# Performance work log

Measured on AMD Instinct MI355X. Metric: run time of the kernel, lower is better.

Reference implementation:

```python
import jax, jax.numpy as jnp
import numpy as np

N = 50000      # nodes
E = 400000     # edges per meta-path
P = 3          # meta-paths
H = 4          # attention heads
D = 32         # hidden_size per head
IN = 128       # in_size = 86 + 42
HD = H * D     # 128
NEG_SLOPE = 0.2


def setup_inputs() -> dict:
    key = jax.random.key(0)
    ks = jax.random.split(key, 13)
    return {
        "h": jax.random.normal(ks[0], (N, 86), dtype=jnp.float32),
        "c_ineigh_feature": jax.random.normal(ks[1], (N, 20, 42), dtype=jnp.float32),
        "fa_w1": jax.random.normal(ks[2], (42, 16), dtype=jnp.float32) * 0.1,
        "fa_b1": jnp.zeros((16,), dtype=jnp.float32),
        "fa_w2": jax.random.normal(ks[3], (16, 1), dtype=jnp.float32) * 0.1,
        "gat_W": jax.random.normal(ks[4], (P, IN, HD), dtype=jnp.float32) * 0.05,
        "attn_l": jax.random.normal(ks[5], (P, H, D), dtype=jnp.float32) * 0.1,
        "attn_r": jax.random.normal(ks[6], (P, H, D), dtype=jnp.float32) * 0.1,
        "sa_w1": jax.random.normal(ks[7], (HD, 128), dtype=jnp.float32) * 0.1,
        "sa_b1": jnp.zeros((128,), dtype=jnp.float32),
        "sa_w2": jax.random.normal(ks[8], (128, 1), dtype=jnp.float32) * 0.1,
        "src": jax.random.randint(ks[9], (P, E), 0, N, dtype=jnp.int32),
        "dst": jax.random.randint(ks[10], (P, E), 0, N, dtype=jnp.int32),
    }


def _gat_conv(x, W, a_l, a_r, s, d):
    """DGL-style GATConv (feat_drop=attn_drop=0, eval mode), activation=elu."""
    feat = (x @ W).reshape(N, H, D)               # [N,H,D]
    el = (feat * a_l).sum(-1)                     # [N,H]
    er = (feat * a_r).sum(-1)                     # [N,H]
    e = el[s] + er[d]                             # [E,H]
    e = jnp.where(e > 0, e, NEG_SLOPE * e)        # leaky_relu(0.2)
    # edge softmax over incoming edges of each dst node
    m = jax.ops.segment_max(e, d, num_segments=N)
    m = jax.lax.stop_gradient(jnp.where(jnp.isfinite(m), m, 0.0))
    ee = jnp.exp(e - m[d])                        # [E,H]
    z = jax.ops.segment_sum(ee, d, num_segments=N)
    alpha = ee / z[d]                             # [E,H]
    msg = alpha[:, :, None] * feat[s]             # [E,H,D]
    out = jax.ops.segment_sum(msg, d, num_segments=N)  # [N,H,D]
    return jax.nn.elu(out).reshape(N, HD)


def reference(h, c_ineigh_feature, fa_w1, fa_b1, fa_w2, gat_W, attn_l, attn_r,
              sa_w1, sa_b1, sa_w2, src, dst):
    # FeatureAttention over the 42-dim neighbor features
    w = jnp.tanh(c_ineigh_feature @ fa_w1 + fa_b1) @ fa_w2   # [N,20,1]
    beta = jax.nn.softmax(w, axis=1)
    c_emb = (beta * c_ineigh_feature).sum(1)                 # [N,42]
    x = jnp.concatenate([h, c_emb], axis=1)                  # [N,128]

    # One GATConv per meta-path
    embs = [_gat_conv(x, gat_W[p], attn_l[p], attn_r[p], src[p], dst[p])
            for p in range(P)]
    z = jnp.stack(embs, axis=1)                              # [N,P,HD]

    # SemanticAttention across meta-paths
    wsem = (jnp.tanh(z @ sa_w1 + sa_b1) @ sa_w2).mean(0)     # [P,1]
    bsem = jax.nn.softmax(wsem, axis=0)                      # [P,1]
    return (bsem[None] * z).sum(1)                           # [N,HD]
```

## Files before the change

kernel.cpp:

```cpp
#include <hip/hip_runtime.h>
#include <hip/hip_bf16.h>

#define NN 50000
#define EE 400000
#define PP 3
#define NBLK 196

__device__ __forceinline__ float eluf(float v) {
    return v > 0.f ? v : (expf(v) - 1.f);
}

__global__ __launch_bounds__(256) void k_featattn(
    const float* __restrict__ h, const float* __restrict__ c,
    const float* __restrict__ w1, const float* __restrict__ b1,
    const float* __restrict__ w2, float* __restrict__ x)
{
    __shared__ float sC[16 * 840];
    __shared__ float sW1[42 * 16];
    __shared__ float sB1[16];
    __shared__ float sW2[16];
    const int tid = threadIdx.x;
    const int n0 = blockIdx.x * 16;

    for (int i = tid; i < 672; i += 256) sW1[i] = w1[i];
    if (tid < 16) { sB1[tid] = b1[tid]; sW2[tid] = w2[tid]; }

    const float4* c4 = (const float4*)(c + (size_t)n0 * 840);
    float4* sC4 = (float4*)sC;
    for (int i = tid; i < 3360; i += 256) sC4[i] = c4[i];
    __syncthreads();

    const int j  = tid & 15;
    const int nn = tid >> 4;
    const float* myC = sC + nn * 840;
    const float bj = sB1[j], w2j = sW2[j];

    float part[20];
    for (int r = 0; r < 20; ++r) {
        float acc = bj;
        const float* row = myC + r * 42;
        #pragma unroll
        for (int i = 0; i < 42; ++i) acc += row[i] * sW1[i * 16 + j];
        part[r] = tanhf(acc) * w2j;
    }
    #pragma unroll
    for (int r = 0; r < 20; ++r) {
        float v = part[r];
        v += __shfl_xor(v, 1);
        v += __shfl_xor(v, 2);
        v += __shfl_xor(v, 4);
        v += __shfl_xor(v, 8);
        part[r] = v;
    }
    float m = part[0];
    #pragma unroll
    for (int r = 1; r < 20; ++r) m = fmaxf(m, part[r]);
    float s = 0.f;
    #pragma unroll
    for (int r = 0; r < 20; ++r) { part[r] = expf(part[r] - m); s += part[r]; }
    const float inv = 1.f / s;

    float e0 = 0.f, e1 = 0.f, e2 = 0.f;
    #pragma unroll
    for (int r = 0; r < 20; ++r) {
        const float b = part[r] * inv;
        const float* row = myC + r * 42;
        e0 += b * row[j];
        e1 += b * row[j + 16];
        if (j < 10) e2 += b * row[j + 32];
    }
    const int n = n0 + nn;
    float* xr = x + (size_t)n * 128;
    xr[86 + j]      = e0;
    xr[86 + j + 16] = e1;
    if (j < 10) xr[86 + j + 32] = e2;

    for (int i = tid; i < 16 * 86; i += 256) {
        const int node = i / 86, col = i % 86;
        x[(size_t)(n0 + node) * 128 + col] = h[(size_t)(n0 + node) * 86 + col];
    }
}

__global__ __launch_bounds__(256) void k_gat_gemm(
    const float* __restrict__ x, const float* __restrict__ W,
    const float* __restrict__ attn_l, const float* __restrict__ attn_r,
    float* __restrict__ feat, float* __restrict__ el, float* __restrict__ er)
{
    __shared__ float sX[64 * 128];
    const int tid = threadIdx.x;
    const int p  = blockIdx.y;
    const int n0 = blockIdx.x * 64;

    float4* sX4 = (float4*)sX;
    for (int i = tid; i < 2048; i += 256) {
        const int row = i >> 5, c4 = i & 31;
        float4 v = make_float4(0.f, 0.f, 0.f, 0.f);
        if (n0 + row < NN) v = ((const float4*)(x + (size_t)(n0 + row) * 128))[c4];
        sX4[i] = v;
    }
    __syncthreads();

    const int tc = tid & 31;
    const int tr = tid >> 5;
    const float* Wp = W + (size_t)p * 128 * 128;

    float acc[8][4];
    for (int r = 0; r < 8; ++r)
        for (int q = 0; q < 4; ++q) acc[r][q] = 0.f;

    #pragma unroll 4
    for (int k = 0; k < 128; ++k) {
        const float4 wv = ((const float4*)(Wp + k * 128))[tc];
        #pragma unroll
        for (int r = 0; r < 8; ++r) {
            const float xv = sX[(tr * 8 + r) * 128 + k];
            acc[r][0] += xv * wv.x;
            acc[r][1] += xv * wv.y;
            acc[r][2] += xv * wv.z;
            acc[r][3] += xv * wv.w;
        }
    }

    float al[4], ar[4];
    {
        const float* alp = attn_l + p * 128 + tc * 4;
        const float* arp = attn_r + p * 128 + tc * 4;
        for (int q = 0; q < 4; ++q) { al[q] = alp[q]; ar[q] = arp[q]; }
    }
    const int hh = tc >> 3;
    for (int r = 0; r < 8; ++r) {
        const int n = n0 + tr * 8 + r;
        const bool ok = n < NN;
        if (ok) {
            const float4 v = make_float4(acc[r][0], acc[r][1], acc[r][2], acc[r][3]);
            ((float4*)(feat + (size_t)(p * NN + n) * 128))[tc] = v;
        }
        float pl = acc[r][0]*al[0] + acc[r][1]*al[1] + acc[r][2]*al[2] + acc[r][3]*al[3];
        float pr = acc[r][0]*ar[0] + acc[r][1]*ar[1] + acc[r][2]*ar[2] + acc[r][3]*ar[3];
        pl += __shfl_xor(pl, 1); pl += __shfl_xor(pl, 2); pl += __shfl_xor(pl, 4);
        pr += __shfl_xor(pr, 1); pr += __shfl_xor(pr, 2); pr += __shfl_xor(pr, 4);
        if (ok && (tc & 7) == 0) {
            el[(size_t)(p * NN + n) * 4 + hh] = pl;
            er[(size_t)(p * NN + n) * 4 + hh] = pr;
        }
    }
}

__global__ __launch_bounds__(256) void k_hist(
    const int* __restrict__ dst, int* __restrict__ deg)
{
    const int p = blockIdx.y;
    const int e = blockIdx.x * 256 + threadIdx.x;
    if (e < EE) atomicAdd(&deg[p * NN + dst[p * EE + e]], 1);
}

__global__ __launch_bounds__(256) void k_partial(
    const int* __restrict__ deg, int* __restrict__ psum)
{
    __shared__ int s[256];
    const int p = blockIdx.y;
    const int i = blockIdx.x * 256 + threadIdx.x;
    s[threadIdx.x] = (i < NN) ? deg[p * NN + i] : 0;
    __syncthreads();
    for (int off = 128; off > 0; off >>= 1) {
        if (threadIdx.x < off) s[threadIdx.x] += s[threadIdx.x + off];
        __syncthreads();
    }
    if (threadIdx.x == 0) psum[p * NBLK + blockIdx.x] = s[0];
}

__global__ void k_scanpsum(int* __restrict__ psum)
{
    const int p = blockIdx.x;
    if (threadIdx.x == 0) {
        int run = 0;
        for (int i = 0; i < NBLK; ++i) {
            int t = psum[p * NBLK + i];
            psum[p * NBLK + i] = run;
            run += t;
        }
    }
}

__global__ __launch_bounds__(256) void k_scanfinal(
    const int* __restrict__ deg, const int* __restrict__ psum,
    int* __restrict__ row_start, int* __restrict__ cursor)
{
    __shared__ int s[256];
    const int p = blockIdx.y, t = threadIdx.x;
    const int i = blockIdx.x * 256 + t;
    const int v = (i < NN) ? deg[p * NN + i] : 0;
    s[t] = v;
    __syncthreads();
    for (int off = 1; off < 256; off <<= 1) {
        int xv = 0;
        if (t >= off) xv = s[t - off];
        __syncthreads();
        s[t] += xv;
        __syncthreads();
    }
    const int excl = s[t] - v + psum[p * NBLK + blockIdx.x];
    if (i < NN) {
        row_start[p * (NN + 1) + i] = excl;
        cursor[p * NN + i] = excl;
        if (i == NN - 1) row_start[p * (NN + 1) + NN] = excl + v;
    }
}

__global__ __launch_bounds__(256) void k_scatter(
    const int* __restrict__ src, const int* __restrict__ dst,
    const float* __restrict__ el, const float* __restrict__ er,
    int* __restrict__ cursor, int* __restrict__ s_src, float* __restrict__ s_ee)
{
    const int p = blockIdx.y;
    const int e = blockIdx.x * 256 + threadIdx.x;
    if (e >= EE) return;
    const int s = src[p * EE + e];
    const int d = dst[p * EE + e];
    const float4 a = ((const float4*)el)[p * NN + s];
    const float4 b = ((const float4*)er)[p * NN + d];
    float4 o;
    {
        float t0 = a.x + b.x, t1 = a.y + b.y, t2 = a.z + b.z, t3 = a.w + b.w;
        t0 = t0 > 0.f ? t0 : 0.2f * t0;
        t1 = t1 > 0.f ? t1 : 0.2f * t1;
        t2 = t2 > 0.f ? t2 : 0.2f * t2;
        t3 = t3 > 0.f ? t3 : 0.2f * t3;
        o = make_float4(expf(t0), expf(t1), expf(t2), expf(t3));
    }
    const int slot = atomicAdd(&cursor[p * NN + d], 1);
    s_src[p * EE + slot] = s;
    ((float4*)s_ee)[p * EE + slot] = o;
}

__global__ __launch_bounds__(256) void k_agg(
    const int* __restrict__ row_start, const int* __restrict__ s_src,
    const float* __restrict__ s_ee, const float* __restrict__ feat,
    float* __restrict__ z)
{
    const int p = blockIdx.y;
    const int w = threadIdx.x >> 6;
    const int lane = threadIdx.x & 63;
    const int n = blockIdx.x * 4 + w;
    if (n >= NN) return;
    const int st = row_start[p * (NN + 1) + n];
    const int en = row_start[p * (NN + 1) + n + 1];

    const bool lo = lane < 32;
    const int* ss = s_src + (size_t)p * EE;
    const float4* ee4 = (const float4*)s_ee + (size_t)p * EE;
    const float* fbase = feat + (size_t)p * NN * 128;

    float acc0 = 0.f, acc1 = 0.f, za = 0.f, zb = 0.f;
    for (int i = st; i < en; ++i) {
        const int sn = ss[i];
        const float4 e4 = ee4[i];
        const float ea = lo ? e4.x : e4.y;
        const float eb = lo ? e4.z : e4.w;
        const float* f = fbase + (size_t)sn * 128;
        acc0 += ea * f[lane];
        acc1 += eb * f[lane + 64];
        za += ea;
        zb += eb;
    }
    float v0 = 0.f, v1 = 0.f;
    if (en > st) { v0 = acc0 / za; v1 = acc1 / zb; }
    v0 = v0 > 0.f ? v0 : (expf(v0) - 1.f);
    v1 = v1 > 0.f ? v1 : (expf(v1) - 1.f);
    const size_t o = (size_t)(p * NN + n) * 128;
    z[o + lane] = v0;
    z[o + 64 + lane] = v1;
}

__global__ __launch_bounds__(256) void k_sem_score(
    const float* __restrict__ z, const float* __restrict__ w1,
    const float* __restrict__ b1, const float* __restrict__ w2,
    float* __restrict__ wsem)
{
    __shared__ float sZ[64 * 128];
    __shared__ float sPart[8];
    const int tid = threadIdx.x;
    const int p  = blockIdx.y;
    const int n0 = blockIdx.x * 64;

    float4* sZ4 = (float4*)sZ;
    for (int i = tid; i < 2048; i += 256) {
        const int row = i >> 5, c4 = i & 31;
        float4 v = make_float4(0.f, 0.f, 0.f, 0.f);
        if (n0 + row < NN)
            v = ((const float4*)(z + (size_t)(p * NN + n0 + row) * 128))[c4];
        sZ4[i] = v;
    }
    __syncthreads();

    const int tc = tid & 31;
    const int tr = tid >> 5;

    float acc[8][4];
    for (int r = 0; r < 8; ++r)
        for (int q = 0; q < 4; ++q) acc[r][q] = 0.f;

    #pragma unroll 4
    for (int k = 0; k < 128; ++k) {
        const float4 wv = ((const float4*)(w1 + k * 128))[tc];
        #pragma unroll
        for (int r = 0; r < 8; ++r) {
            const float zv = sZ[(tr * 8 + r) * 128 + k];
            acc[r][0] += zv * wv.x;
            acc[r][1] += zv * wv.y;
            acc[r][2] += zv * wv.z;
            acc[r][3] += zv * wv.w;
        }
    }

    float bb[4], ww[4];
    for (int q = 0; q < 4; ++q) { bb[q] = b1[tc * 4 + q]; ww[q] = w2[tc * 4 + q]; }

    float local = 0.f;
    for (int r = 0; r < 8; ++r) {
        float pr = 0.f;
        for (int q = 0; q < 4; ++q) pr += tanhf(acc[r][q] + bb[q]) * ww[q];
        pr += __shfl_xor(pr, 1);
        pr += __shfl_xor(pr, 2);
        pr += __shfl_xor(pr, 4);
        pr += __shfl_xor(pr, 8);
        pr += __shfl_xor(pr, 16);
        if (tc == 0 && (n0 + tr * 8 + r) < NN) local += pr;
    }
    if (tc == 0) sPart[tr] = local;
    __syncthreads();
    if (tid == 0) {
        float t = 0.f;
        for (int i = 0; i < 8; ++i) t += sPart[i];
        atomicAdd(&wsem[p], t);
    }
}

__global__ void k_bsem(const float* __restrict__ wsem, float* __restrict__ bsem)
{
    if (threadIdx.x == 0 && blockIdx.x == 0) {
        float w[PP];
        for (int p = 0; p < PP; ++p) w[p] = wsem[p] / (float)NN;
        float m = fmaxf(w[0], fmaxf(w[1], w[2]));
        float s = 0.f;
        for (int p = 0; p < PP; ++p) { w[p] = expf(w[p] - m); s += w[p]; }
        for (int p = 0; p < PP; ++p) bsem[p] = w[p] / s;
    }
}

__global__ __launch_bounds__(256) void k_final(
    const float* __restrict__ z, const float* __restrict__ bsem,
    float* __restrict__ out)
{
    const int i = blockIdx.x * 256 + threadIdx.x;
    if (i >= NN * 128) return;
    const float b0 = bsem[0], b1 = bsem[1], b2 = bsem[2];
    const float v0 = z[i];
    const float v1 = z[(size_t)NN * 128 + i];
    const float v2 = z[(size_t)2 * NN * 128 + i];
    out[i] = b0 * v0 + b1 * v1 + b2 * v2;
}

extern "C" void kernel_launch(void* const* d_in, const int* in_sizes, int n_in,
                              void* d_out, int out_size, void* d_ws, size_t ws_size,
                              hipStream_t stream) {
    const float* h      = (const float*)d_in[0];
    const float* c      = (const float*)d_in[1];
    const float* fa_w1  = (const float*)d_in[2];
    const float* fa_b1  = (const float*)d_in[3];
    const float* fa_w2  = (const float*)d_in[4];
    const float* gat_W  = (const float*)d_in[5];
    const float* attn_l = (const float*)d_in[6];
    const float* attn_r = (const float*)d_in[7];
    const float* sa_w1  = (const float*)d_in[8];
    const float* sa_b1  = (const float*)d_in[9];
    const float* sa_w2  = (const float*)d_in[10];
    const int*   src    = (const int*)d_in[11];
    const int*   dst    = (const int*)d_in[12];
    float* out = (float*)d_out;

    float* ws = (float*)d_ws;
    float* x    = ws;
    int*   s_src = (int*)x;
    float* s_ee  = x + 1200000;
    float* feat = x + 6400000;
    float* el   = feat + 19200000;
    float* er   = el + 600000;
    float* z    = er + 600000;
    int*   row_start = (int*)(z + 19200000);
    int*   cursor    = row_start + 150003;
    int*   psum      = cursor + 150000;
    int*   deg       = psum + 588;
    float* wsem      = (float*)(deg + 150000);
    float* bsem      = wsem + 4;

    hipMemsetAsync(deg, 0, (size_t)(150000 + 4) * sizeof(float), stream);

    k_featattn<<<NN / 16, 256, 0, stream>>>(h, c, fa_w1, fa_b1, fa_w2, x);
    k_gat_gemm<<<dim3((NN + 63) / 64, PP), 256, 0, stream>>>(x, gat_W, attn_l, attn_r, feat, el, er);
    k_hist<<<dim3((EE + 255) / 256, PP), 256, 0, stream>>>(dst, deg);
    k_partial<<<dim3(NBLK, PP), 256, 0, stream>>>(deg, psum);
    k_scanpsum<<<PP, 64, 0, stream>>>(psum);
    k_scanfinal<<<dim3(NBLK, PP), 256, 0, stream>>>(deg, psum, row_start, cursor);
    k_scatter<<<dim3((EE + 255) / 256, PP), 256, 0, stream>>>(src, dst, el, er, cursor, s_src, s_ee);
    k_agg<<<dim3((NN + 3) / 4, PP), 256, 0, stream>>>(row_start, s_src, s_ee, feat, z);
    k_sem_score<<<dim3((NN + 63) / 64, PP), 256, 0, stream>>>(z, sa_w1, sa_b1, sa_w2, wsem);
    k_bsem<<<1, 64, 0, stream>>>(wsem, bsem);
    k_final<<<(NN * 128 + 255) / 256, 256, 0, stream>>>(z, bsem, out);
}
```

Baseline: 817.4 us.

## Store GAT features in bf16, split feature attention, vectorize GEMM inner loops

GAT projected features are rounded to bf16 on write and gathered as packed pairs in the aggregation kernel, halving the bytes read per edge; each lane now covers two adjacent columns of one head. Feature attention is split into a per-row score kernel with register tiling and a per-node softmax/embedding kernel, removing the large shared-memory staging of the neighbor tensor. The projection and semantic-score GEMMs read shared memory as float4 and unroll over k by four. Precision loss from bf16 features may slightly change outputs.

```diff
diff --git a/kernel.cpp b/kernel.cpp
--- a/kernel.cpp
+++ b/kernel.cpp
@@ -10,81 +10,117 @@
     return v > 0.f ? v : (expf(v) - 1.f);
 }
 
-__global__ __launch_bounds__(256) void k_featattn(
+__device__ __forceinline__ void fma4(float4& a, float s, const float4& w) {
+    a.x += s * w.x; a.y += s * w.y; a.z += s * w.z; a.w += s * w.w;
+}
+
+__device__ __forceinline__ unsigned short f2bf(float f) {
+    unsigned int u = __float_as_uint(f);
+    u = (u + 0x7FFFu + ((u >> 16) & 1u)) >> 16;
+    return (unsigned short)u;
+}
+
+__global__ __launch_bounds__(256) void k_fa_w(
+    const float* __restrict__ c, const float* __restrict__ w1,
+    const float* __restrict__ b1, const float* __restrict__ w2,
+    float* __restrict__ wout)
+{
+    __shared__ float sW1[42 * 16];
+    const int tid = threadIdx.x;
+    for (int i = tid; i < 672; i += 256) sW1[i] = w1[i];
+    __syncthreads();
+
+    const int t = blockIdx.x * 256 + tid;
+    if (t >= NN * 5) return;
+    const int n = t / 5;
+    const int q = t - 5 * n;
+
+    const float2* base = (const float2*)(c + (size_t)n * 840 + q * 168);
+    const float4* sW4 = (const float4*)sW1;
+
+    float4 acc[4][4];
+    #pragma unroll
+    for (int r = 0; r < 4; ++r)
+        #pragma unroll
+        for (int jq = 0; jq < 4; ++jq) acc[r][jq] = make_float4(0.f, 0.f, 0.f, 0.f);
+
+    #pragma unroll 3
+    for (int i2 = 0; i2 < 21; ++i2) {
+        const float4 wa0 = sW4[(2 * i2) * 4 + 0];
+        const float4 wa1 = sW4[(2 * i2) * 4 + 1];
+        const float4 wa2 = sW4[(2 * i2) * 4 + 2];
+        const float4 wa3 = sW4[(2 * i2) * 4 + 3];
+        const float4 wb0 = sW4[(2 * i2 + 1) * 4 + 0];
+        const float4 wb1 = sW4[(2 * i2 + 1) * 4 + 1];
+        const float4 wb2 = sW4[(2 * i2 + 1) * 4 + 2];
+        const float4 wb3 = sW4[(2 * i2 + 1) * 4 + 3];
+        #pragma unroll
+        for (int r = 0; r < 4; ++r) {
+            const float2 v = base[r * 21 + i2];
+            fma4(acc[r][0], v.x, wa0); fma4(acc[r][1], v.x, wa1);
+            fma4(acc[r][2], v.x, wa2); fma4(acc[r][3], v.x, wa3);
+            fma4(acc[r][0], v.y, wb0); fma4(acc[r][1], v.y, wb1);
+            fma4(acc[r][2], v.y, wb2); fma4(acc[r][3], v.y, wb3);
+        }
+    }
+
+    float4 bb[4], ww[4];
+    #pragma unroll
+    for (int jq = 0; jq < 4; ++jq) {
+        bb[jq] = ((const float4*)b1)[jq];
+        ww[jq] = ((const float4*)w2)[jq];
+    }
+    float* wo = wout + (size_t)n * 20 + q * 4;
+    #pragma unroll
+    for (int r = 0; r < 4; ++r) {
+        float s = 0.f;
+        #pragma unroll
+        for (int jq = 0; jq < 4; ++jq) {
+            s += tanhf(acc[r][jq].x + bb[jq].x) * ww[jq].x;
+            s += tanhf(acc[r][jq].y + bb[jq].y) * ww[jq].y;
+            s += tanhf(acc[r][jq].z + bb[jq].z) * ww[jq].z;
+            s += tanhf(acc[r][jq].w + bb[jq].w) * ww[jq].w;
+        }
+        wo[r] = s;
+    }
+}
+
+__global__ __launch_bounds__(256) void k_fa_emb(
     const float* __restrict__ h, const float* __restrict__ c,
-    const float* __restrict__ w1, const float* __restrict__ b1,
-    const float* __restrict__ w2, float* __restrict__ x)
-{
-    __shared__ float sC[16 * 840];
-    __shared__ float sW1[42 * 16];
-    __shared__ float sB1[16];
-    __shared__ float sW2[16];
-    const int tid = threadIdx.x;
-    const int n0 = blockIdx.x * 16;
-
-    for (int i = tid; i < 672; i += 256) sW1[i] = w1[i];
-    if (tid < 16) { sB1[tid] = b1[tid]; sW2[tid] = w2[tid]; }
-
-    const float4* c4 = (const float4*)(c + (size_t)n0 * 840);
-    float4* sC4 = (float4*)sC;
-    for (int i = tid; i < 3360; i += 256) sC4[i] = c4[i];
-    __syncthreads();
-
-    const int j  = tid & 15;
-    const int nn = tid >> 4;
-    const float* myC = sC + nn * 840;
-    const float bj = sB1[j], w2j = sW2[j];
-
-    float part[20];
-    for (int r = 0; r < 20; ++r) {
-        float acc = bj;
-        const float* row = myC + r * 42;
-        #pragma unroll
-        for (int i = 0; i < 42; ++i) acc += row[i] * sW1[i * 16 + j];
-        part[r] = tanhf(acc) * w2j;
-    }
-    #pragma unroll
-    for (int r = 0; r < 20; ++r) {
-        float v = part[r];
-        v += __shfl_xor(v, 1);
-        v += __shfl_xor(v, 2);
-        v += __shfl_xor(v, 4);
-        v += __shfl_xor(v, 8);
-        part[r] = v;
-    }
-    float m = part[0];
-    #pragma unroll
-    for (int r = 1; r < 20; ++r) m = fmaxf(m, part[r]);
+    const float* __restrict__ w, float* __restrict__ x)
+{
+    const int wid = threadIdx.x >> 6, lane = threadIdx.x & 63;
+    const int n = blockIdx.x * 4 + wid;
+    if (n >= NN) return;
+
+    const float* wn = w + (size_t)n * 20;
+    float wv[20];
+    #pragma unroll
+    for (int r = 0; r < 20; ++r) wv[r] = wn[r];
+    float m = wv[0];
+    #pragma unroll
+    for (int r = 1; r < 20; ++r) m = fmaxf(m, wv[r]);
     float s = 0.f;
     #pragma unroll
-    for (int r = 0; r < 20; ++r) { part[r] = expf(part[r] - m); s += part[r]; }
+    for (int r = 0; r < 20; ++r) { wv[r] = expf(wv[r] - m); s += wv[r]; }
     const float inv = 1.f / s;
 
-    float e0 = 0.f, e1 = 0.f, e2 = 0.f;
-    #pragma unroll
-    for (int r = 0; r < 20; ++r) {
-        const float b = part[r] * inv;
-        const float* row = myC + r * 42;
-        e0 += b * row[j];
-        e1 += b * row[j + 16];
-        if (j < 10) e2 += b * row[j + 32];
-    }
-    const int n = n0 + nn;
-    float* xr = x + (size_t)n * 128;
-    xr[86 + j]      = e0;
-    xr[86 + j + 16] = e1;
-    if (j < 10) xr[86 + j + 32] = e2;
-
-    for (int i = tid; i < 16 * 86; i += 256) {
-        const int node = i / 86, col = i % 86;
-        x[(size_t)(n0 + node) * 128 + col] = h[(size_t)(n0 + node) * 86 + col];
-    }
+    if (lane < 42) {
+        const float* cn = c + (size_t)n * 840;
+        float acc = 0.f;
+        #pragma unroll
+        for (int r = 0; r < 20; ++r) acc += wv[r] * cn[r * 42 + lane];
+        x[(size_t)n * 128 + 86 + lane] = acc * inv;
+    }
+    x[(size_t)n * 128 + lane] = h[(size_t)n * 86 + lane];
+    if (lane < 22)
+        x[(size_t)n * 128 + 64 + lane] = h[(size_t)n * 86 + 64 + lane];
 }
 
 __global__ __launch_bounds__(256) void k_gat_gemm(
     const float* __restrict__ x, const float* __restrict__ W,
     const float* __restrict__ attn_l, const float* __restrict__ attn_r,
-    float* __restrict__ feat, float* __restrict__ el, float* __restrict__ er)
+    unsigned short* __restrict__ featb, float* __restrict__ el, float* __restrict__ er)
 {
     __shared__ float sX[64 * 128];
     const int tid = threadIdx.x;
@@ -102,41 +138,44 @@
 
     const int tc = tid & 31;
     const int tr = tid >> 5;
-    const float* Wp = W + (size_t)p * 128 * 128;
-
-    float acc[8][4];
-    for (int r = 0; r < 8; ++r)
-        for (int q = 0; q < 4; ++q) acc[r][q] = 0.f;
-
-    #pragma unroll 4
-    for (int k = 0; k < 128; ++k) {
-        const float4 wv = ((const float4*)(Wp + k * 128))[tc];
+    const float4* Wp4 = (const float4*)(W + (size_t)p * 128 * 128);
+
+    float4 acc[8];
+    #pragma unroll
+    for (int r = 0; r < 8; ++r) acc[r] = make_float4(0.f, 0.f, 0.f, 0.f);
+
+    for (int kq = 0; kq < 32; ++kq) {
+        const float4 wv0 = Wp4[(4 * kq + 0) * 32 + tc];
+        const float4 wv1 = Wp4[(4 * kq + 1) * 32 + tc];
+        const float4 wv2 = Wp4[(4 * kq + 2) * 32 + tc];
+        const float4 wv3 = Wp4[(4 * kq + 3) * 32 + tc];
         #pragma unroll
         for (int r = 0; r < 8; ++r) {
-            const float xv = sX[(tr * 8 + r) * 128 + k];
-            acc[r][0] += xv * wv.x;
-            acc[r][1] += xv * wv.y;
-            acc[r][2] += xv * wv.z;
-            acc[r][3] += xv * wv.w;
-        }
-    }
-
-    float al[4], ar[4];
+            const float4 xv = sX4[(tr * 8 + r) * 32 + kq];
+            fma4(acc[r], xv.x, wv0);
+            fma4(acc[r], xv.y, wv1);
+            fma4(acc[r], xv.z, wv2);
+            fma4(acc[r], xv.w, wv3);
+        }
+    }
+
+    float4 al, ar;
     {
-        const float* alp = attn_l + p * 128 + tc * 4;
-        const float* arp = attn_r + p * 128 + tc * 4;
-        for (int q = 0; q < 4; ++q) { al[q] = alp[q]; ar[q] = arp[q]; }
+        al = ((const float4*)(attn_l + p * 128))[tc];
+        ar = ((const float4*)(attn_r + p * 128))[tc];
     }
     const int hh = tc >> 3;
     for (int r = 0; r < 8; ++r) {
         const int n = n0 + tr * 8 + r;
         const bool ok = n < NN;
         if (ok) {
-            const float4 v = make_float4(acc[r][0], acc[r][1], acc[r][2], acc[r][3]);
-            ((float4*)(feat + (size_t)(p * NN + n) * 128))[tc] = v;
-        }
-        float pl = acc[r][0]*al[0] + acc[r][1]*al[1] + acc[r][2]*al[2] + acc[r][3]*al[3];
-        float pr = acc[r][0]*ar[0] + acc[r][1]*ar[1] + acc[r][2]*ar[2] + acc[r][3]*ar[3];
+            ushort4 sv;
+            sv.x = f2bf(acc[r].x); sv.y = f2bf(acc[r].y);
+            sv.z = f2bf(acc[r].z); sv.w = f2bf(acc[r].w);
+            ((ushort4*)(featb + (size_t)(p * NN + n) * 128))[tc] = sv;
+        }
+        float pl = acc[r].x*al.x + acc[r].y*al.y + acc[r].z*al.z + acc[r].w*al.w;
+        float pr = acc[r].x*ar.x + acc[r].y*ar.y + acc[r].z*ar.z + acc[r].w*ar.w;
         pl += __shfl_xor(pl, 1); pl += __shfl_xor(pl, 2); pl += __shfl_xor(pl, 4);
         pr += __shfl_xor(pr, 1); pr += __shfl_xor(pr, 2); pr += __shfl_xor(pr, 4);
         if (ok && (tc & 7) == 0) {
@@ -235,7 +274,7 @@
 
 __global__ __launch_bounds__(256) void k_agg(
     const int* __restrict__ row_start, const int* __restrict__ s_src,
-    const float* __restrict__ s_ee, const float* __restrict__ feat,
+    const float* __restrict__ s_ee, const unsigned short* __restrict__ featb,
     float* __restrict__ z)
 {
     const int p = blockIdx.y;
@@ -246,30 +285,29 @@
     const int st = row_start[p * (NN + 1) + n];
     const int en = row_start[p * (NN + 1) + n + 1];
 
-    const bool lo = lane < 32;
+    const int h = lane >> 4;
     const int* ss = s_src + (size_t)p * EE;
     const float4* ee4 = (const float4*)s_ee + (size_t)p * EE;
-    const float* fbase = feat + (size_t)p * NN * 128;
-
-    float acc0 = 0.f, acc1 = 0.f, za = 0.f, zb = 0.f;
+    const unsigned short* fbase = featb + (size_t)p * NN * 128;
+
+    float acc0 = 0.f, acc1 = 0.f, za = 0.f;
     for (int i = st; i < en; ++i) {
         const int sn = ss[i];
         const float4 e4 = ee4[i];
-        const float ea = lo ? e4.x : e4.y;
-        const float eb = lo ? e4.z : e4.w;
-        const float* f = fbase + (size_t)sn * 128;
-        acc0 += ea * f[lane];
-        acc1 += eb * f[lane + 64];
+        const float ea = (h < 2) ? (h == 0 ? e4.x : e4.y) : (h == 2 ? e4.z : e4.w);
+        const unsigned int u = ((const unsigned int*)(fbase + (size_t)sn * 128))[lane];
+        const float f0 = __uint_as_float(u << 16);
+        const float f1 = __uint_as_float(u & 0xFFFF0000u);
+        acc0 += ea * f0;
+        acc1 += ea * f1;
         za += ea;
-        zb += eb;
     }
     float v0 = 0.f, v1 = 0.f;
-    if (en > st) { v0 = acc0 / za; v1 = acc1 / zb; }
+    if (en > st) { const float iz = 1.f / za; v0 = acc0 * iz; v1 = acc1 * iz; }
     v0 = v0 > 0.f ? v0 : (expf(v0) - 1.f);
     v1 = v1 > 0.f ? v1 : (expf(v1) - 1.f);
     const size_t o = (size_t)(p * NN + n) * 128;
-    z[o + lane] = v0;
-    z[o + 64 + lane] = v1;
+    ((float2*)(z + o))[lane] = make_float2(v0, v1);
 }
 
 __global__ __launch_bounds__(256) void k_sem_score(
@@ -295,31 +333,36 @@
 
     const int tc = tid & 31;
     const int tr = tid >> 5;
-
-    float acc[8][4];
-    for (int r = 0; r < 8; ++r)
-        for (int q = 0; q < 4; ++q) acc[r][q] = 0.f;
-
-    #pragma unroll 4
-    for (int k = 0; k < 128; ++k) {
-        const float4 wv = ((const float4*)(w1 + k * 128))[tc];
+    const float4* w14 = (const float4*)w1;
+
+    float4 acc[8];
+    #pragma unroll
+    for (int r = 0; r < 8; ++r) acc[r] = make_float4(0.f, 0.f, 0.f, 0.f);
+
+    for (int kq = 0; kq < 32; ++kq) {
+        const float4 wv0 = w14[(4 * kq + 0) * 32 + tc];
+        const float4 wv1 = w14[(4 * kq + 1) * 32 + tc];
+        const float4 wv2 = w14[(4 * kq + 2) * 32 + tc];
+        const float4 wv3 = w14[(4 * kq + 3) * 32 + tc];
         #pragma unroll
         for (int r = 0; r < 8; ++r) {
-            const float zv = sZ[(tr * 8 + r) * 128 + k];
-            acc[r][0] += zv * wv.x;
-            acc[r][1] += zv * wv.y;
-            acc[r][2] += zv * wv.z;
-            acc[r][3] += zv * wv.w;
-        }
-    }
-
-    float bb[4], ww[4];
-    for (int q = 0; q < 4; ++q) { bb[q] = b1[tc * 4 + q]; ww[q] = w2[tc * 4 + q]; }
+            const float4 zv = sZ4[(tr * 8 + r) * 32 + kq];
+            fma4(acc[r], zv.x, wv0);
+            fma4(acc[r], zv.y, wv1);
+            fma4(acc[r], zv.z, wv2);
+            fma4(acc[r], zv.w, wv3);
+        }
+    }
+
+    const float4 bb = ((const float4*)b1)[tc];
+    const float4 ww = ((const float4*)w2)[tc];
 
     float local = 0.f;
     for (int r = 0; r < 8; ++r) {
-        float pr = 0.f;
-        for (int q = 0; q < 4; ++q) pr += tanhf(acc[r][q] + bb[q]) * ww[q];
+        float pr = tanhf(acc[r].x + bb.x) * ww.x
+                 + tanhf(acc[r].y + bb.y) * ww.y
+                 + tanhf(acc[r].z + bb.z) * ww.z
+                 + tanhf(acc[r].w + bb.w) * ww.w;
         pr += __shfl_xor(pr, 1);
         pr += __shfl_xor(pr, 2);
         pr += __shfl_xor(pr, 4);
@@ -380,13 +423,14 @@
     float* out = (float*)d_out;
 
     float* ws = (float*)d_ws;
-    float* x    = ws;
-    int*   s_src = (int*)x;
-    float* s_ee  = x + 1200000;
-    float* feat = x + 6400000;
-    float* el   = feat + 19200000;
-    float* er   = el + 600000;
-    float* z    = er + 600000;
+    float* x     = ws;
+    int*   s_src = (int*)ws;
+    float* s_ee  = ws + 1200000;
+    float* w_fa  = ws + 6400000;
+    unsigned short* featb = (unsigned short*)(ws + 7400000);
+    float* el    = ws + 17000000;
+    float* er    = el + 600000;
+    float* z     = er + 600000;
     int*   row_start = (int*)(z + 19200000);
     int*   cursor    = row_start + 150003;
     int*   psum      = cursor + 150000;
@@ -396,14 +440,15 @@
 
     hipMemsetAsync(deg, 0, (size_t)(150000 + 4) * sizeof(float), stream);
 
-    k_featattn<<<NN / 16, 256, 0, stream>>>(h, c, fa_w1, fa_b1, fa_w2, x);
-    k_gat_gemm<<<dim3((NN + 63) / 64, PP), 256, 0, stream>>>(x, gat_W, attn_l, attn_r, feat, el, er);
+    k_fa_w<<<(NN * 5 + 255) / 256, 256, 0, stream>>>(c, fa_w1, fa_b1, fa_w2, w_fa);
+    k_fa_emb<<<(NN + 3) / 4, 256, 0, stream>>>(h, c, w_fa, x);
+    k_gat_gemm<<<dim3((NN + 63) / 64, PP), 256, 0, stream>>>(x, gat_W, attn_l, attn_r, featb, el, er);
     k_hist<<<dim3((EE + 255) / 256, PP), 256, 0, stream>>>(dst, deg);
     k_partial<<<dim3(NBLK, PP), 256, 0, stream>>>(deg, psum);
     k_scanpsum<<<PP, 64, 0, stream>>>(psum);
     k_scanfinal<<<dim3(NBLK, PP), 256, 0, stream>>>(deg, psum, row_start, cursor);
     k_scatter<<<dim3((EE + 255) / 256, PP), 256, 0, stream>>>(src, dst, el, er, cursor, s_src, s_ee);
-    k_agg<<<dim3((NN + 3) / 4, PP), 256, 0, stream>>>(row_start, s_src, s_ee, feat, z);
+    k_agg<<<dim3((NN + 3) / 4, PP), 256, 0, stream>>>(row_start, s_src, s_ee, featb, z);
     k_sem_score<<<dim3((NN + 63) / 64, PP), 256, 0, stream>>>(z, sa_w1, sa_b1, sa_w2, wsem);
     k_bsem<<<1, 64, 0, stream>>>(wsem, bsem);
     k_final<<<(NN * 128 + 255) / 256, 256, 0, stream>>>(z, bsem, out);
```

After: 912.8 us. +11.7%, slower.
